# Optimization experiments

Hardware: AMD Instinct MI355X
Metric: run time of the kernel (lower is better)

The kernel has to match this reference:

```python
import jax, jax.numpy as jnp
import numpy as np

BLANK_ID = 0

def setup_inputs() -> dict:
    key = jax.random.key(0)
    k1, k2, k3, k4 = jax.random.split(key, 4)
    B, T, U, V = 4, 512, 100, 1024
    logits = jax.random.normal(k1, (B, T, U + 1, V), dtype=jnp.float32)
    labels = jax.random.randint(k2, (B, U), 0, V, dtype=jnp.int32)
    logit_lengths = jax.random.randint(k3, (B,), 0, T, dtype=jnp.int32)
    label_lengths = jax.random.randint(k4, (B,), 0, U, dtype=jnp.int32)
    return {"logits": logits, "labels": labels,
            "logit_lengths": logit_lengths, "label_lengths": label_lengths}


def _rnnt_alpha_final(logits, labels, logit_lengths, label_lengths):
    # logits: (B, T, U+1, V) treated as log-probs (as in the torch CPU path)
    B, T, Up1, V = logits.shape
    U = Up1 - 1
    dt = logits.dtype

    blank = logits[..., BLANK_ID]                                   # (B, T, U+1)
    # emit[b,t,u] = logits[b,t,u,labels[b,u]] for u in [0,U)
    emit = jnp.take_along_axis(logits[:, :, :U, :],
                               labels[:, None, :, None], axis=3)[..., 0]  # (B, T, U)

    zero_col = jnp.zeros((B, 1), dtype=dt)
    # Row t=0: alpha[0,u] = sum_{j<u} emit[0,j], alpha[0,0] = 0
    row0 = jnp.concatenate([zero_col, jnp.cumsum(emit[:, 0, :], axis=1)], axis=1)  # (B, U+1)

    def step(prev, xs):
        # prev: alpha row at t-1, shape (B, U+1)
        blank_tm1, emit_t = xs   # (B, U+1), (B, U)
        # Recurrence: row[u] = logaddexp(prev[u] + blank_tm1[u], row[u-1] + emit_t[u-1])
        # Linear log-domain recurrence solved with cumulative logsumexp:
        #   row[u] = C[u] + logcumsumexp(a - C)[u], a = prev + blank_tm1, C = prefix-sum of emit_t
        a = prev + blank_tm1
        C = jnp.concatenate([zero_col, jnp.cumsum(emit_t, axis=1)], axis=1)  # (B, U+1)
        row = C + jax.lax.cumlogsumexp(a - C, axis=1)
        return row, row

    xs = (jnp.swapaxes(blank[:, :-1, :], 0, 1),   # blank at t-1, for t = 1..T-1
          jnp.swapaxes(emit[:, 1:, :], 0, 1))     # emit at t,   for t = 1..T-1
    _, rows = jax.lax.scan(step, row0, xs)        # (T-1, B, U+1)
    alpha = jnp.concatenate([row0[None], rows], axis=0)  # (T, B, U+1)

    t_idx = logit_lengths - 1                     # alpha[T_b - 1, :]
    u_idx = label_lengths                         # column U_b
    per_sample = -alpha[t_idx, jnp.arange(B), u_idx]
    return per_sample


def reference(logits, labels, logit_lengths, label_lengths):
    V = logits.shape[-1]
    logit_lengths = jnp.clip(logit_lengths, 1, logits.shape[1])
    label_lengths = jnp.clip(label_lengths, 1, logits.shape[2] - 1)
    labels = jnp.clip(labels, 0, V - 1)
    per_sample = _rnnt_alpha_final(logits, labels, logit_lengths, label_lengths)
    # reduction = 'mean': sum over batch / batch_size, returned with shape (1,)
    return jnp.mean(per_sample).reshape(1)
```

## Files before the change

### kernel.cpp

```cpp
#include <hip/hip_runtime.h>


constexpr int B = 4, T = 512, U = 100, Up1 = 101, V = 1024;
constexpr int DIAGS = T + U;
constexpr int MM4 = (DIAGS + 3) / 4;
constexpr int W = 4;
constexpr float LOG2E = 1.44269504088896340736f;
constexpr float LN2 = 0.69314718055994530942f;

__device__ double2 g_D1[(size_t)B * MM4 * 64];
__device__ double2 g_D2[(size_t)B * MM4 * 64];
__device__ double2 g_D3[(size_t)B * MM4 * 64];
__device__ double2 g_D4[(size_t)B * MM4 * 64];
__device__ double2 g_D5[(size_t)B * MM4 * 64];
__device__ double2 g_L1[3][B * 64];
__device__ double2 g_L2[3][B * 64];
__device__ float g_mm[B * MM4];
__device__ float g_lastm[B][3];
__device__ float g_ps[B];
__device__ int g_ctr = 0;

__device__ __forceinline__ int clampi(int x, int lo, int hi) {
  return x < lo ? lo : (x > hi ? hi : x);
}
__device__ __forceinline__ float fexp2(float x) {
  float r; asm("v_exp_f32 %0, %1" : "=v"(r) : "v"(x)); return r;
}
__device__ __forceinline__ float flog2(float x) {
  float r; asm("v_log_f32 %0, %1" : "=v"(r) : "v"(x)); return r;
}
__device__ __forceinline__ double wave_shr1_f64(double x) {
  int hi = __double2hiint(x), lo = __double2loint(x);
  hi = __builtin_amdgcn_update_dpp(hi, hi, 0x138 , 0xF, 0xF, false);
  lo = __builtin_amdgcn_update_dpp(lo, lo, 0x138 , 0xF, 0xF, false);
  return __hiloint2double(hi, lo);
}

__global__ __launch_bounds__(256) void gather_kernel(const float* __restrict__ logits,
                                                     const int* __restrict__ labels,
                                                     const int* __restrict__ logit_len,
                                                     const int* __restrict__ label_len) {
  const int b = blockIdx.y;
  const int mr = blockIdx.x * 4 + (threadIdx.x >> 6);
  const int l = threadIdx.x & 63;
  if (mr >= MM4) return;
  const int Tb = clampi(logit_len[b], 1, T);
  const int Ub = clampi(label_len[b], 1, U);
  const int smax = Tb - 1 + Ub;
  const int Mq = smax >> 2, rem = smax & 3;

  const float* lg = logits + (size_t)b * T * Up1 * V;
  const int u0 = 2 * l, u1 = u0 + 1;
  int labz = 0, labw = 0;
  if (u0 >= 1 && u0 <= U) labz = clampi(labels[b * U + (u0 - 1)], 0, V - 1);
  if (u0 < U)             labw = clampi(labels[b * U + u0], 0, V - 1);

  if (mr >= Mq) {
    const size_t idx = ((size_t)b * MM4 + mr) * 64 + l;
    g_D1[idx] = make_double2(1.0, 0.0);
    g_D2[idx] = make_double2(0.0, 0.0);
    g_D3[idx] = make_double2(0.0, 1.0);
    g_D4[idx] = make_double2(0.0, 0.0);
    g_D5[idx] = make_double2(0.0, 0.0);
    if (l == 0) g_mm[b * MM4 + mr] = 0.f;

    if (mr == Mq) {
      for (int j = 0; j < rem; ++j) {
        int r = 4 * Mq + j;
        float vx = 0.f, vy = 0.f, vz = 0.f, vw = 0.f;
        bool bx = false, by = false, bz = false, bw = false;
        int tx = r - u0;
        if (u0 <= Ub && tx >= 0 && tx <= Tb - 1) { vx = LOG2E * lg[((size_t)tx * Up1 + u0) * V]; bx = true; }
        int ty = r - u1;
        if (u1 <= Ub && ty >= 0 && ty <= Tb - 1) { vy = LOG2E * lg[((size_t)ty * Up1 + u1) * V]; by = true; }
        int tz = r - u0 + 1;
        if (u0 >= 1 && u0 <= Ub && tz >= 0 && tz <= Tb - 1) { vz = LOG2E * lg[((size_t)tz * Up1 + (u0 - 1)) * V + labz]; bz = true; }
        int tw = r - u0;
        if (u0 <= Ub - 1 && tw >= 0 && tw <= Tb - 1) { vw = LOG2E * lg[((size_t)tw * Up1 + u0) * V + labw]; bw = true; }
        float s_ = (bx ? vx : 0.f) + (by ? vy : 0.f) + (bz ? vz : 0.f) + (bw ? vw : 0.f);
        float c_ = (float)((int)bx + (int)by + (int)bz + (int)bw);
        for (int off = 32; off; off >>= 1) { s_ += __shfl_xor(s_, off, 64); c_ += __shfl_xor(c_, off, 64); }
        float m = (c_ > 0.f) ? rintf(s_ / c_) : 0.f;
        g_L1[j][b * 64 + l] = make_double2(bx ? (double)fexp2(vx - m) : 0.0,
                                           bz ? (double)fexp2(vz - m) : 0.0);
        g_L2[j][b * 64 + l] = make_double2(by ? (double)fexp2(vy - m) : 0.0,
                                           bw ? (double)fexp2(vw - m) : 0.0);
        if (l == 0) g_lastm[b][j] = m;
      }
    }
    return;
  }

  float vx[4], vy[4], vz[4], vw[4];
  bool bx[4], by[4], bz[4], bw[4];
#pragma unroll
  for (int k = 0; k < 4; ++k) {
    int r = 4 * mr + k;
    vx[k] = vy[k] = vz[k] = vw[k] = 0.f;
    bx[k] = by[k] = bz[k] = bw[k] = false;
    int tx = r - u0;
    if (u0 <= Ub && tx >= 0 && tx <= Tb - 1) { vx[k] = LOG2E * lg[((size_t)tx * Up1 + u0) * V]; bx[k] = true; }
    int ty = r - u1;
    if (u1 <= Ub && ty >= 0 && ty <= Tb - 1) { vy[k] = LOG2E * lg[((size_t)ty * Up1 + u1) * V]; by[k] = true; }
    int tz = r - u0 + 1;
    if (u0 >= 1 && u0 <= Ub && tz >= 0 && tz <= Tb - 1) { vz[k] = LOG2E * lg[((size_t)tz * Up1 + (u0 - 1)) * V + labz]; bz[k] = true; }
    int tw = r - u0;
    if (u0 <= Ub - 1 && tw >= 0 && tw <= Tb - 1) { vw[k] = LOG2E * lg[((size_t)tw * Up1 + u0) * V + labw]; bw[k] = true; }
  }
  float s_ = 0.f, c_ = 0.f;
#pragma unroll
  for (int k = 0; k < 4; ++k) {
    s_ += (bx[k] ? vx[k] : 0.f) + (by[k] ? vy[k] : 0.f) +
          (bz[k] ? vz[k] : 0.f) + (bw[k] ? vw[k] : 0.f);
    c_ += (float)((int)bx[k] + (int)by[k] + (int)bz[k] + (int)bw[k]);
  }
  for (int off = 32; off; off >>= 1) { s_ += __shfl_xor(s_, off, 64); c_ += __shfl_xor(c_, off, 64); }
  const float m = (c_ > 0.f) ? rintf(s_ / c_) : 0.f;

  float fX[4], fY[4], fZ[4], fW[4];
#pragma unroll
  for (int k = 0; k < 4; ++k) {
    fX[k] = bx[k] ? fexp2(vx[k] - m) : 0.f;
    fY[k] = by[k] ? fexp2(vy[k] - m) : 0.f;
    fZ[k] = bz[k] ? fexp2(vz[k] - m) : 0.f;
    fW[k] = bw[k] ? fexp2(vw[k] - m) : 0.f;
  }

#define COMP2(P, Q, R_, S, Tc, Uc, i, jj)                                      \
  {                                                                            \
    float y1n = __shfl_up(fY[i], 1, 64);                                       \
    float w1n = __shfl_up(fW[i], 1, 64);                                       \
    double X1 = fX[i], Y1 = fY[i], Z1 = fZ[i], W1 = fW[i];                     \
    double X2 = fX[jj], Y2 = fY[jj], Z2 = fZ[jj], W2 = fW[jj];                 \
    P = X2 * X1; Q = X2 * Z1 + Z2 * (double)y1n; R_ = Z2 * (double)w1n;        \
    S = Y2 * Y1; Tc = W2 * X1 + Y2 * W1; Uc = W2 * Z1;                         \
  }
  double Mp, Mq_, Mr, Ms, Mt, Mu, Np, Nq, Nr, Ns, Nt, Nu;
  COMP2(Mp, Mq_, Mr, Ms, Mt, Mu, 0, 1);
  COMP2(Np, Nq, Nr, Ns, Nt, Nu, 2, 3);
#undef COMP2
  double Mp1 = __shfl_up(Mp, 1, 64), Mq1 = __shfl_up(Mq_, 1, 64);
  double Mr1 = __shfl_up(Mr, 1, 64), Ms1 = __shfl_up(Ms, 1, 64);
  double Mt1 = __shfl_up(Mt, 1, 64), Mu1 = __shfl_up(Mu, 1, 64);

  double dA  = Np * Mp;
  double dB1 = Np * Mq_ + Nq * Ms1;
  double dA1 = Np * Mr + Nq * Mt1 + Nr * Mp1;
  double dB2 = Nq * Mu1 + Nr * Mq1;
  double dA2 = Nr * Mr1;
  double eB  = Ns * Ms;
  double eA  = Ns * Mt + Nt * Mp;
  double eB1 = Ns * Mu + Nt * Mq_ + Nu * Ms1;
  double eA1 = Nt * Mr + Nu * Mt1;
  double eB2 = Nu * Mu1;

  const size_t idx = ((size_t)b * MM4 + mr) * 64 + l;
  g_D1[idx] = make_double2(dA, dB1);
  g_D2[idx] = make_double2(dA1, dB2);
  g_D3[idx] = make_double2(dA2, eB);
  g_D4[idx] = make_double2(eA, eB1);
  g_D5[idx] = make_double2(eA1, eB2);
  if (l == 0) g_mm[b * MM4 + mr] = 4.f * m;
}

__global__ __launch_bounds__(64, 1)
void dp_kernel(const int* __restrict__ logit_len,
               const int* __restrict__ label_len,
               float* __restrict__ out) {
  const int b = blockIdx.x;
  const int lane = threadIdx.x;
  const int Tb = clampi(logit_len[b], 1, T);
  const int Ub = clampi(label_len[b], 1, U);
  const int smax = Tb - 1 + Ub;
  const int Mq = smax >> 2, rem = smax & 3;
  const double2* D1 = g_D1 + (size_t)b * MM4 * 64 + lane;
  const double2* D2 = g_D2 + (size_t)b * MM4 * 64 + lane;
  const double2* D3 = g_D3 + (size_t)b * MM4 * 64 + lane;
  const double2* D4 = g_D4 + (size_t)b * MM4 * 64 + lane;
  const double2* D5 = g_D5 + (size_t)b * MM4 * 64 + lane;

  double A = (lane == 0) ? 1.0 : 0.0;
  double Bc = 0.0;

  double2 a1[W], a2[W], a3[W], a4[W], a5[W];
  double2 b1[W], b2[W], b3[W], b4[W], b5[W];
  double2 c1[W], c2[W], c3[W], c4[W], c5[W];

#define LOADG(u1_, u2_, u3_, u4_, u5_, grp)                                    \
  {                                                                            \
    const size_t o_ = (size_t)(grp) * (W * 64);                                \
    _Pragma("unroll")                                                          \
    for (int j_ = 0; j_ < W; ++j_) {                                           \
      u1_[j_] = D1[o_ + j_ * 64];                                              \
      u2_[j_] = D2[o_ + j_ * 64];                                              \
      u3_[j_] = D3[o_ + j_ * 64];                                              \
      u4_[j_] = D4[o_ + j_ * 64];                                              \
      u5_[j_] = D5[o_ + j_ * 64];                                              \
    }                                                                          \
  }

#define STEPS(u1_, u2_, u3_, u4_, u5_)                                         \
  {                                                                            \
    _Pragma("unroll")                                                          \
    for (int j_ = 0; j_ < W; ++j_) {                                           \
      double A1s = wave_shr1_f64(A);                                           \
      double B1s = wave_shr1_f64(Bc);                                          \
      double A2s = wave_shr1_f64(A1s);                                         \
      double B2s = wave_shr1_f64(B1s);                                         \
      double na = fma(A, u1_[j_].x, fma(B1s, u1_[j_].y,                        \
                   fma(A1s, u2_[j_].x, fma(B2s, u2_[j_].y,                     \
                       A2s * u3_[j_].x))));                                    \
      double nb = fma(Bc, u3_[j_].y, fma(A, u4_[j_].x,                         \
                   fma(B1s, u4_[j_].y, fma(A1s, u5_[j_].x,                     \
                       B2s * u5_[j_].y))));                                    \
      A = na; Bc = nb;                                                         \
    }                                                                          \
  }

  const int NWC = (Mq + W - 1) / W;
  if (NWC > 0) {
    LOADG(a1, a2, a3, a4, a5, 0);
    if (NWC > 1) LOADG(b1, b2, b3, b4, b5, 1);
    for (int k = 0; k < NWC; k += 3) {
      if (k + 2 < NWC) LOADG(c1, c2, c3, c4, c5, k + 2);
      STEPS(a1, a2, a3, a4, a5);
      if (k + 1 < NWC) {
        if (k + 3 < NWC) LOADG(a1, a2, a3, a4, a5, k + 3);
        STEPS(b1, b2, b3, b4, b5);
        if (k + 2 < NWC) {
          if (k + 4 < NWC) LOADG(b1, b2, b3, b4, b5, k + 4);
          STEPS(c1, c2, c3, c4, c5);
        }
      }
    }
  }
  for (int j = 0; j < rem; ++j) {
    double2 L1 = g_L1[j][b * 64 + lane];
    double2 L2 = g_L2[j][b * 64 + lane];
    double shrB = wave_shr1_f64(Bc);
    double na = fma(A, L1.x, shrB * L1.y);
    double nb = fma(Bc, L2.x, A * L2.y);
    A = na; Bc = nb;
  }

  const int ansLane = Ub >> 1;
  double va = __shfl(A, ansLane, 64);
  double vb = __shfl(Bc, ansLane, 64);
  double v = (Ub & 1) ? vb : va;
  int ev = ((__double2hiint(v) >> 20) & 0x7ff) - 1023;
  double mant = ldexp(v, -ev);

  float msum = 0.f;
  for (int mI = lane; mI < Mq; mI += 64) msum += g_mm[b * MM4 + mI];
  for (int off = 32; off; off >>= 1) msum += __shfl_xor(msum, off, 64);
  for (int j = 0; j < rem; ++j) msum += g_lastm[b][j];

  float lg2 = (float)ev + flog2((float)mant) + msum;

  if (lane == 0) {
    __hip_atomic_store(&g_ps[b], lg2, __ATOMIC_RELEASE, __HIP_MEMORY_SCOPE_AGENT);
    int old = __hip_atomic_fetch_add(&g_ctr, 1, __ATOMIC_ACQ_REL,
                                     __HIP_MEMORY_SCOPE_AGENT);
    if (old == B - 1) {
      float s = 0.0f;
      for (int i = 0; i < B; ++i)
        s += __hip_atomic_load(&g_ps[i], __ATOMIC_ACQUIRE, __HIP_MEMORY_SCOPE_AGENT);
      out[0] = -s * (LN2 / B);
      __hip_atomic_store(&g_ctr, 0, __ATOMIC_RELAXED, __HIP_MEMORY_SCOPE_AGENT);
    }
  }
#undef LOADG
#undef STEPS
}

extern "C" void kernel_launch(void* const* d_in, const int* in_sizes, int n_in,
                              void* d_out, int out_size, void* d_ws, size_t ws_size,
                              hipStream_t stream) {
  const float* logits = (const float*)d_in[0];
  const int* labels = (const int*)d_in[1];
  const int* logit_len = (const int*)d_in[2];
  const int* label_len = (const int*)d_in[3];
  float* out = (float*)d_out;

  hipLaunchKernelGGL(gather_kernel, dim3((MM4 + 3) / 4, B), dim3(256), 0, stream,
                     logits, labels, logit_len, label_len);
  hipLaunchKernelGGL(dp_kernel, dim3(B), dim3(64), 0, stream,
                     logit_len, label_len, out);
}
```

Measured before the change: 30.42 us.

## Compose eight anti-diagonal transfer steps per matrix in gather kernel

The gather kernel now multiplies two 4-step banded transfer operators into one 8-step operator, so each wave stores nine double2 coefficient arrays per eight diagonals instead of five per four. The sequential DP kernel then runs half as many dependent steps, each using wider shifts (up to four lanes) and a tree-shaped sum instead of an FMA chain. This shortens the serial critical path at the cost of more DPP shifts and multiplies per step, more register pressure from the prefetch buffers, and a larger remainder of up to seven single steps.

```diff
diff --git a/kernel.cpp b/kernel.cpp
--- a/kernel.cpp
+++ b/kernel.cpp
@@ -3,20 +3,24 @@
 
 constexpr int B = 4, T = 512, U = 100, Up1 = 101, V = 1024;
 constexpr int DIAGS = T + U;
-constexpr int MM4 = (DIAGS + 3) / 4;
-constexpr int W = 4;
+constexpr int MM8 = 78;
+constexpr int W = 3;
 constexpr float LOG2E = 1.44269504088896340736f;
 constexpr float LN2 = 0.69314718055994530942f;
 
-__device__ double2 g_D1[(size_t)B * MM4 * 64];
-__device__ double2 g_D2[(size_t)B * MM4 * 64];
-__device__ double2 g_D3[(size_t)B * MM4 * 64];
-__device__ double2 g_D4[(size_t)B * MM4 * 64];
-__device__ double2 g_D5[(size_t)B * MM4 * 64];
-__device__ double2 g_L1[3][B * 64];
-__device__ double2 g_L2[3][B * 64];
-__device__ float g_mm[B * MM4];
-__device__ float g_lastm[B][3];
+__device__ double2 g_G1[(size_t)B * MM8 * 64];
+__device__ double2 g_G2[(size_t)B * MM8 * 64];
+__device__ double2 g_G3[(size_t)B * MM8 * 64];
+__device__ double2 g_G4[(size_t)B * MM8 * 64];
+__device__ double2 g_G5[(size_t)B * MM8 * 64];
+__device__ double2 g_G6[(size_t)B * MM8 * 64];
+__device__ double2 g_G7[(size_t)B * MM8 * 64];
+__device__ double2 g_G8[(size_t)B * MM8 * 64];
+__device__ double2 g_G9[(size_t)B * MM8 * 64];
+__device__ double2 g_L1[7][B * 64];
+__device__ double2 g_L2[7][B * 64];
+__device__ float g_mm[B * MM8];
+__device__ float g_lastm[B][7];
 __device__ float g_ps[B];
 __device__ int g_ctr = 0;
 
@@ -43,11 +47,11 @@
   const int b = blockIdx.y;
   const int mr = blockIdx.x * 4 + (threadIdx.x >> 6);
   const int l = threadIdx.x & 63;
-  if (mr >= MM4) return;
+  if (mr >= MM8) return;
   const int Tb = clampi(logit_len[b], 1, T);
   const int Ub = clampi(label_len[b], 1, U);
   const int smax = Tb - 1 + Ub;
-  const int Mq = smax >> 2, rem = smax & 3;
+  const int Mq8 = smax >> 3, rem = smax & 7;
 
   const float* lg = logits + (size_t)b * T * Up1 * V;
   const int u0 = 2 * l, u1 = u0 + 1;
@@ -55,28 +59,37 @@
   if (u0 >= 1 && u0 <= U) labz = clampi(labels[b * U + (u0 - 1)], 0, V - 1);
   if (u0 < U)             labw = clampi(labels[b * U + u0], 0, V - 1);
 
-  if (mr >= Mq) {
-    const size_t idx = ((size_t)b * MM4 + mr) * 64 + l;
-    g_D1[idx] = make_double2(1.0, 0.0);
-    g_D2[idx] = make_double2(0.0, 0.0);
-    g_D3[idx] = make_double2(0.0, 1.0);
-    g_D4[idx] = make_double2(0.0, 0.0);
-    g_D5[idx] = make_double2(0.0, 0.0);
-    if (l == 0) g_mm[b * MM4 + mr] = 0.f;
-
-    if (mr == Mq) {
+#define RAWROW(r, vx, vy, vz, vw, bx, by, bz, bw)                              \
+  {                                                                            \
+    vx = vy = vz = vw = 0.f; bx = by = bz = bw = false;                        \
+    int tx = (r) - u0;                                                         \
+    if (u0 <= Ub && tx >= 0 && tx <= Tb - 1) { vx = LOG2E * lg[((size_t)tx * Up1 + u0) * V]; bx = true; } \
+    int ty = (r) - u1;                                                         \
+    if (u1 <= Ub && ty >= 0 && ty <= Tb - 1) { vy = LOG2E * lg[((size_t)ty * Up1 + u1) * V]; by = true; } \
+    int tz = (r) - u0 + 1;                                                     \
+    if (u0 >= 1 && u0 <= Ub && tz >= 0 && tz <= Tb - 1) { vz = LOG2E * lg[((size_t)tz * Up1 + (u0 - 1)) * V + labz]; bz = true; } \
+    int tw = (r) - u0;                                                         \
+    if (u0 <= Ub - 1 && tw >= 0 && tw <= Tb - 1) { vw = LOG2E * lg[((size_t)tw * Up1 + u0) * V + labw]; bw = true; } \
+  }
+
+  if (mr >= Mq8) {
+    const size_t idx = ((size_t)b * MM8 + mr) * 64 + l;
+    g_G1[idx] = make_double2(1.0, 0.0);
+    g_G2[idx] = make_double2(0.0, 0.0);
+    g_G3[idx] = make_double2(0.0, 0.0);
+    g_G4[idx] = make_double2(0.0, 0.0);
+    g_G5[idx] = make_double2(0.0, 0.0);
+    g_G6[idx] = make_double2(0.0, 0.0);
+    g_G7[idx] = make_double2(0.0, 1.0);
+    g_G8[idx] = make_double2(0.0, 0.0);
+    g_G9[idx] = make_double2(0.0, 0.0);
+    if (l == 0) g_mm[b * MM8 + mr] = 0.f;
+
+    if (mr == Mq8) {
       for (int j = 0; j < rem; ++j) {
-        int r = 4 * Mq + j;
-        float vx = 0.f, vy = 0.f, vz = 0.f, vw = 0.f;
-        bool bx = false, by = false, bz = false, bw = false;
-        int tx = r - u0;
-        if (u0 <= Ub && tx >= 0 && tx <= Tb - 1) { vx = LOG2E * lg[((size_t)tx * Up1 + u0) * V]; bx = true; }
-        int ty = r - u1;
-        if (u1 <= Ub && ty >= 0 && ty <= Tb - 1) { vy = LOG2E * lg[((size_t)ty * Up1 + u1) * V]; by = true; }
-        int tz = r - u0 + 1;
-        if (u0 >= 1 && u0 <= Ub && tz >= 0 && tz <= Tb - 1) { vz = LOG2E * lg[((size_t)tz * Up1 + (u0 - 1)) * V + labz]; bz = true; }
-        int tw = r - u0;
-        if (u0 <= Ub - 1 && tw >= 0 && tw <= Tb - 1) { vw = LOG2E * lg[((size_t)tw * Up1 + u0) * V + labw]; bw = true; }
+        int r = 8 * Mq8 + j;
+        float vx, vy, vz, vw; bool bx, by, bz, bw;
+        RAWROW(r, vx, vy, vz, vw, bx, by, bz, bw);
         float s_ = (bx ? vx : 0.f) + (by ? vy : 0.f) + (bz ? vz : 0.f) + (bw ? vw : 0.f);
         float c_ = (float)((int)bx + (int)by + (int)bz + (int)bw);
         for (int off = 32; off; off >>= 1) { s_ += __shfl_xor(s_, off, 64); c_ += __shfl_xor(c_, off, 64); }
@@ -91,25 +104,15 @@
     return;
   }
 
-  float vx[4], vy[4], vz[4], vw[4];
-  bool bx[4], by[4], bz[4], bw[4];
+  float vx[8], vy[8], vz[8], vw[8];
+  bool bx[8], by[8], bz[8], bw[8];
 #pragma unroll
-  for (int k = 0; k < 4; ++k) {
-    int r = 4 * mr + k;
-    vx[k] = vy[k] = vz[k] = vw[k] = 0.f;
-    bx[k] = by[k] = bz[k] = bw[k] = false;
-    int tx = r - u0;
-    if (u0 <= Ub && tx >= 0 && tx <= Tb - 1) { vx[k] = LOG2E * lg[((size_t)tx * Up1 + u0) * V]; bx[k] = true; }
-    int ty = r - u1;
-    if (u1 <= Ub && ty >= 0 && ty <= Tb - 1) { vy[k] = LOG2E * lg[((size_t)ty * Up1 + u1) * V]; by[k] = true; }
-    int tz = r - u0 + 1;
-    if (u0 >= 1 && u0 <= Ub && tz >= 0 && tz <= Tb - 1) { vz[k] = LOG2E * lg[((size_t)tz * Up1 + (u0 - 1)) * V + labz]; bz[k] = true; }
-    int tw = r - u0;
-    if (u0 <= Ub - 1 && tw >= 0 && tw <= Tb - 1) { vw[k] = LOG2E * lg[((size_t)tw * Up1 + u0) * V + labw]; bw[k] = true; }
-  }
+  for (int k = 0; k < 8; ++k)
+    RAWROW(8 * mr + k, vx[k], vy[k], vz[k], vw[k], bx[k], by[k], bz[k], bw[k]);
+
   float s_ = 0.f, c_ = 0.f;
 #pragma unroll
-  for (int k = 0; k < 4; ++k) {
+  for (int k = 0; k < 8; ++k) {
     s_ += (bx[k] ? vx[k] : 0.f) + (by[k] ? vy[k] : 0.f) +
           (bz[k] ? vz[k] : 0.f) + (bw[k] ? vw[k] : 0.f);
     c_ += (float)((int)bx[k] + (int)by[k] + (int)bz[k] + (int)bw[k]);
@@ -117,9 +120,9 @@
   for (int off = 32; off; off >>= 1) { s_ += __shfl_xor(s_, off, 64); c_ += __shfl_xor(c_, off, 64); }
   const float m = (c_ > 0.f) ? rintf(s_ / c_) : 0.f;
 
-  float fX[4], fY[4], fZ[4], fW[4];
+  float fX[8], fY[8], fZ[8], fW[8];
 #pragma unroll
-  for (int k = 0; k < 4; ++k) {
+  for (int k = 0; k < 8; ++k) {
     fX[k] = bx[k] ? fexp2(vx[k] - m) : 0.f;
     fY[k] = by[k] ? fexp2(vy[k] - m) : 0.f;
     fZ[k] = bz[k] ? fexp2(vz[k] - m) : 0.f;
@@ -135,32 +138,77 @@
     P = X2 * X1; Q = X2 * Z1 + Z2 * (double)y1n; R_ = Z2 * (double)w1n;        \
     S = Y2 * Y1; Tc = W2 * X1 + Y2 * W1; Uc = W2 * Z1;                         \
   }
-  double Mp, Mq_, Mr, Ms, Mt, Mu, Np, Nq, Nr, Ns, Nt, Nu;
-  COMP2(Mp, Mq_, Mr, Ms, Mt, Mu, 0, 1);
-  COMP2(Np, Nq, Nr, Ns, Nt, Nu, 2, 3);
+#define COMP4(aa0, aa1, aa2, ab1, ab2, ba0, ba1, bb0, bb1, bb2, i0)            \
+  {                                                                            \
+    double Mp, Mq_, Mr, Ms, Mt, Mu, Np, Nq, Nr, Ns, Nt, Nu;                    \
+    COMP2(Mp, Mq_, Mr, Ms, Mt, Mu, (i0), (i0) + 1);                            \
+    COMP2(Np, Nq, Nr, Ns, Nt, Nu, (i0) + 2, (i0) + 3);                         \
+    double Mp1 = __shfl_up(Mp, 1, 64), Mq1 = __shfl_up(Mq_, 1, 64);            \
+    double Mr1 = __shfl_up(Mr, 1, 64), Ms1 = __shfl_up(Ms, 1, 64);             \
+    double Mt1 = __shfl_up(Mt, 1, 64), Mu1 = __shfl_up(Mu, 1, 64);             \
+    aa0 = Np * Mp;                                                             \
+    ab1 = Np * Mq_ + Nq * Ms1;                                                 \
+    aa1 = Np * Mr + Nq * Mt1 + Nr * Mp1;                                       \
+    ab2 = Nq * Mu1 + Nr * Mq1;                                                 \
+    aa2 = Nr * Mr1;                                                            \
+    bb0 = Ns * Ms;                                                             \
+    ba0 = Ns * Mt + Nt * Mp;                                                   \
+    bb1 = Ns * Mu + Nt * Mq_ + Nu * Ms1;                                       \
+    ba1 = Nt * Mr + Nu * Mt1;                                                  \
+    bb2 = Nu * Mu1;                                                            \
+  }
+
+  double Maa0, Maa1, Maa2, Mab1, Mab2, Mba0, Mba1, Mbb0, Mbb1, Mbb2;
+  double Naa0, Naa1, Naa2, Nab1, Nab2, Nba0, Nba1, Nbb0, Nbb1, Nbb2;
+  COMP4(Maa0, Maa1, Maa2, Mab1, Mab2, Mba0, Mba1, Mbb0, Mbb1, Mbb2, 0);
+  COMP4(Naa0, Naa1, Naa2, Nab1, Nab2, Nba0, Nba1, Nbb0, Nbb1, Nbb2, 4);
+#undef COMP4
 #undef COMP2
-  double Mp1 = __shfl_up(Mp, 1, 64), Mq1 = __shfl_up(Mq_, 1, 64);
-  double Mr1 = __shfl_up(Mr, 1, 64), Ms1 = __shfl_up(Ms, 1, 64);
-  double Mt1 = __shfl_up(Mt, 1, 64), Mu1 = __shfl_up(Mu, 1, 64);
-
-  double dA  = Np * Mp;
-  double dB1 = Np * Mq_ + Nq * Ms1;
-  double dA1 = Np * Mr + Nq * Mt1 + Nr * Mp1;
-  double dB2 = Nq * Mu1 + Nr * Mq1;
-  double dA2 = Nr * Mr1;
-  double eB  = Ns * Ms;
-  double eA  = Ns * Mt + Nt * Mp;
-  double eB1 = Ns * Mu + Nt * Mq_ + Nu * Ms1;
-  double eA1 = Nt * Mr + Nu * Mt1;
-  double eB2 = Nu * Mu1;
-
-  const size_t idx = ((size_t)b * MM4 + mr) * 64 + l;
-  g_D1[idx] = make_double2(dA, dB1);
-  g_D2[idx] = make_double2(dA1, dB2);
-  g_D3[idx] = make_double2(dA2, eB);
-  g_D4[idx] = make_double2(eA, eB1);
-  g_D5[idx] = make_double2(eA1, eB2);
-  if (l == 0) g_mm[b * MM4 + mr] = 4.f * m;
+
+  double sMaa0_1 = __shfl_up(Maa0, 1, 64), sMaa0_2 = __shfl_up(Maa0, 2, 64);
+  double sMaa1_1 = __shfl_up(Maa1, 1, 64), sMaa1_2 = __shfl_up(Maa1, 2, 64);
+  double sMaa2_1 = __shfl_up(Maa2, 1, 64), sMaa2_2 = __shfl_up(Maa2, 2, 64);
+  double sMab1_1 = __shfl_up(Mab1, 1, 64), sMab1_2 = __shfl_up(Mab1, 2, 64);
+  double sMab2_1 = __shfl_up(Mab2, 1, 64), sMab2_2 = __shfl_up(Mab2, 2, 64);
+  double sMba0_1 = __shfl_up(Mba0, 1, 64), sMba0_2 = __shfl_up(Mba0, 2, 64);
+  double sMba1_1 = __shfl_up(Mba1, 1, 64), sMba1_2 = __shfl_up(Mba1, 2, 64);
+  double sMbb0_1 = __shfl_up(Mbb0, 1, 64), sMbb0_2 = __shfl_up(Mbb0, 2, 64);
+  double sMbb1_1 = __shfl_up(Mbb1, 1, 64), sMbb1_2 = __shfl_up(Mbb1, 2, 64);
+  double sMbb2_1 = __shfl_up(Mbb2, 1, 64), sMbb2_2 = __shfl_up(Mbb2, 2, 64);
+
+  double Paa0 = Naa0 * Maa0;
+  double Paa1 = Naa0 * Maa1 + Naa1 * sMaa0_1 + Nab1 * sMba0_1;
+  double Paa2 = Naa0 * Maa2 + Naa1 * sMaa1_1 + Naa2 * sMaa0_2 +
+                Nab1 * sMba1_1 + Nab2 * sMba0_2;
+  double Paa3 = Naa1 * sMaa2_1 + Naa2 * sMaa1_2 + Nab2 * sMba1_2;
+  double Paa4 = Naa2 * sMaa2_2;
+  double Pab1 = Naa0 * Mab1 + Nab1 * sMbb0_1;
+  double Pab2 = Naa0 * Mab2 + Naa1 * sMab1_1 + Nab1 * sMbb1_1 + Nab2 * sMbb0_2;
+  double Pab3 = Naa1 * sMab2_1 + Naa2 * sMab1_2 + Nab1 * sMbb2_1 + Nab2 * sMbb1_2;
+  double Pab4 = Naa2 * sMab2_2 + Nab2 * sMbb2_2;
+  double Pba0 = Nba0 * Maa0 + Nbb0 * Mba0;
+  double Pba1 = Nba0 * Maa1 + Nba1 * sMaa0_1 + Nbb0 * Mba1 + Nbb1 * sMba0_1;
+  double Pba2 = Nba0 * Maa2 + Nba1 * sMaa1_1 + Nbb1 * sMba1_1 + Nbb2 * sMba0_2;
+  double Pba3 = Nba1 * sMaa2_1 + Nbb2 * sMba1_2;
+  double Pbb0 = Nbb0 * Mbb0;
+  double Pbb1 = Nba0 * Mab1 + Nbb0 * Mbb1 + Nbb1 * sMbb0_1;
+  double Pbb2 = Nba0 * Mab2 + Nba1 * sMab1_1 + Nbb0 * Mbb2 + Nbb1 * sMbb1_1 +
+                Nbb2 * sMbb0_2;
+  double Pbb3 = Nba1 * sMab2_1 + Nbb1 * sMbb2_1 + Nbb2 * sMbb1_2;
+  double Pbb4 = Nbb2 * sMbb2_2;
+
+  const size_t idx = ((size_t)b * MM8 + mr) * 64 + l;
+  g_G1[idx] = make_double2(Paa0, Paa1);
+  g_G2[idx] = make_double2(Paa2, Paa3);
+  g_G3[idx] = make_double2(Paa4, Pab1);
+  g_G4[idx] = make_double2(Pab2, Pab3);
+  g_G5[idx] = make_double2(Pab4, Pba0);
+  g_G6[idx] = make_double2(Pba1, Pba2);
+  g_G7[idx] = make_double2(Pba3, Pbb0);
+  g_G8[idx] = make_double2(Pbb1, Pbb2);
+  g_G9[idx] = make_double2(Pbb3, Pbb4);
+  if (l == 0) g_mm[b * MM8 + mr] = 8.f * m;
+#undef RAWROW
 }
 
 __global__ __launch_bounds__(64, 1)
@@ -172,34 +220,38 @@
   const int Tb = clampi(logit_len[b], 1, T);
   const int Ub = clampi(label_len[b], 1, U);
   const int smax = Tb - 1 + Ub;
-  const int Mq = smax >> 2, rem = smax & 3;
-  const double2* D1 = g_D1 + (size_t)b * MM4 * 64 + lane;
-  const double2* D2 = g_D2 + (size_t)b * MM4 * 64 + lane;
-  const double2* D3 = g_D3 + (size_t)b * MM4 * 64 + lane;
-  const double2* D4 = g_D4 + (size_t)b * MM4 * 64 + lane;
-  const double2* D5 = g_D5 + (size_t)b * MM4 * 64 + lane;
+  const int Mq8 = smax >> 3, rem = smax & 7;
+  const double2* G1 = g_G1 + (size_t)b * MM8 * 64 + lane;
+  const double2* G2 = g_G2 + (size_t)b * MM8 * 64 + lane;
+  const double2* G3 = g_G3 + (size_t)b * MM8 * 64 + lane;
+  const double2* G4 = g_G4 + (size_t)b * MM8 * 64 + lane;
+  const double2* G5 = g_G5 + (size_t)b * MM8 * 64 + lane;
+  const double2* G6 = g_G6 + (size_t)b * MM8 * 64 + lane;
+  const double2* G7 = g_G7 + (size_t)b * MM8 * 64 + lane;
+  const double2* G8 = g_G8 + (size_t)b * MM8 * 64 + lane;
+  const double2* G9 = g_G9 + (size_t)b * MM8 * 64 + lane;
 
   double A = (lane == 0) ? 1.0 : 0.0;
   double Bc = 0.0;
 
-  double2 a1[W], a2[W], a3[W], a4[W], a5[W];
-  double2 b1[W], b2[W], b3[W], b4[W], b5[W];
-  double2 c1[W], c2[W], c3[W], c4[W], c5[W];
-
-#define LOADG(u1_, u2_, u3_, u4_, u5_, grp)                                    \
+  double2 a1[W], a2[W], a3[W], a4[W], a5[W], a6[W], a7[W], a8[W], a9[W];
+  double2 b1[W], b2[W], b3[W], b4[W], b5[W], b6[W], b7[W], b8[W], b9[W];
+  double2 c1[W], c2[W], c3[W], c4[W], c5[W], c6[W], c7[W], c8[W], c9[W];
+
+#define LOADG(u1_, u2_, u3_, u4_, u5_, u6_, u7_, u8_, u9_, grp)                \
   {                                                                            \
     const size_t o_ = (size_t)(grp) * (W * 64);                                \
     _Pragma("unroll")                                                          \
     for (int j_ = 0; j_ < W; ++j_) {                                           \
-      u1_[j_] = D1[o_ + j_ * 64];                                              \
-      u2_[j_] = D2[o_ + j_ * 64];                                              \
-      u3_[j_] = D3[o_ + j_ * 64];                                              \
-      u4_[j_] = D4[o_ + j_ * 64];                                              \
-      u5_[j_] = D5[o_ + j_ * 64];                                              \
+      u1_[j_] = G1[o_ + j_ * 64]; u2_[j_] = G2[o_ + j_ * 64];                  \
+      u3_[j_] = G3[o_ + j_ * 64]; u4_[j_] = G4[o_ + j_ * 64];                  \
+      u5_[j_] = G5[o_ + j_ * 64]; u6_[j_] = G6[o_ + j_ * 64];                  \
+      u7_[j_] = G7[o_ + j_ * 64]; u8_[j_] = G8[o_ + j_ * 64];                  \
+      u9_[j_] = G9[o_ + j_ * 64];                                              \
     }                                                                          \
   }
 
-#define STEPS(u1_, u2_, u3_, u4_, u5_)                                         \
+#define STEPS(u1_, u2_, u3_, u4_, u5_, u6_, u7_, u8_, u9_)                     \
   {                                                                            \
     _Pragma("unroll")                                                          \
     for (int j_ = 0; j_ < W; ++j_) {                                           \
@@ -207,29 +259,37 @@
       double B1s = wave_shr1_f64(Bc);                                          \
       double A2s = wave_shr1_f64(A1s);                                         \
       double B2s = wave_shr1_f64(B1s);                                         \
-      double na = fma(A, u1_[j_].x, fma(B1s, u1_[j_].y,                        \
-                   fma(A1s, u2_[j_].x, fma(B2s, u2_[j_].y,                     \
-                       A2s * u3_[j_].x))));                                    \
-      double nb = fma(Bc, u3_[j_].y, fma(A, u4_[j_].x,                         \
-                   fma(B1s, u4_[j_].y, fma(A1s, u5_[j_].x,                     \
-                       B2s * u5_[j_].y))));                                    \
+      double A3s = wave_shr1_f64(A2s);                                         \
+      double B3s = wave_shr1_f64(B2s);                                         \
+      double A4s = wave_shr1_f64(A3s);                                         \
+      double B4s = wave_shr1_f64(B3s);                                         \
+      double na = ((A * u1_[j_].x + A1s * u1_[j_].y) +                         \
+                   (A2s * u2_[j_].x + A3s * u2_[j_].y)) +                      \
+                  ((A4s * u3_[j_].x + B1s * u3_[j_].y) +                       \
+                   (B2s * u4_[j_].x + B3s * u4_[j_].y)) +                      \
+                  B4s * u5_[j_].x;                                             \
+      double nb = ((A * u5_[j_].y + A1s * u6_[j_].x) +                         \
+                   (A2s * u6_[j_].y + A3s * u7_[j_].x)) +                      \
+                  ((Bc * u7_[j_].y + B1s * u8_[j_].x) +                        \
+                   (B2s * u8_[j_].y + B3s * u9_[j_].x)) +                      \
+                  B4s * u9_[j_].y;                                             \
       A = na; Bc = nb;                                                         \
     }                                                                          \
   }
 
-  const int NWC = (Mq + W - 1) / W;
+  const int NWC = (Mq8 + W - 1) / W;
   if (NWC > 0) {
-    LOADG(a1, a2, a3, a4, a5, 0);
-    if (NWC > 1) LOADG(b1, b2, b3, b4, b5, 1);
+    LOADG(a1, a2, a3, a4, a5, a6, a7, a8, a9, 0);
+    if (NWC > 1) LOADG(b1, b2, b3, b4, b5, b6, b7, b8, b9, 1);
     for (int k = 0; k < NWC; k += 3) {
-      if (k + 2 < NWC) LOADG(c1, c2, c3, c4, c5, k + 2);
-      STEPS(a1, a2, a3, a4, a5);
+      if (k + 2 < NWC) LOADG(c1, c2, c3, c4, c5, c6, c7, c8, c9, k + 2);
+      STEPS(a1, a2, a3, a4, a5, a6, a7, a8, a9);
       if (k + 1 < NWC) {
-        if (k + 3 < NWC) LOADG(a1, a2, a3, a4, a5, k + 3);
-        STEPS(b1, b2, b3, b4, b5);
+        if (k + 3 < NWC) LOADG(a1, a2, a3, a4, a5, a6, a7, a8, a9, k + 3);
+        STEPS(b1, b2, b3, b4, b5, b6, b7, b8, b9);
         if (k + 2 < NWC) {
-          if (k + 4 < NWC) LOADG(b1, b2, b3, b4, b5, k + 4);
-          STEPS(c1, c2, c3, c4, c5);
+          if (k + 4 < NWC) LOADG(b1, b2, b3, b4, b5, b6, b7, b8, b9, k + 4);
+          STEPS(c1, c2, c3, c4, c5, c6, c7, c8, c9);
         }
       }
     }
@@ -251,7 +311,7 @@
   double mant = ldexp(v, -ev);
 
   float msum = 0.f;
-  for (int mI = lane; mI < Mq; mI += 64) msum += g_mm[b * MM4 + mI];
+  for (int mI = lane; mI < Mq8; mI += 64) msum += g_mm[b * MM8 + mI];
   for (int off = 32; off; off >>= 1) msum += __shfl_xor(msum, off, 64);
   for (int j = 0; j < rem; ++j) msum += g_lastm[b][j];
 
@@ -282,7 +342,7 @@
   const int* label_len = (const int*)d_in[3];
   float* out = (float*)d_out;
 
-  hipLaunchKernelGGL(gather_kernel, dim3((MM4 + 3) / 4, B), dim3(256), 0, stream,
+  hipLaunchKernelGGL(gather_kernel, dim3((MM8 + 3) / 4, B), dim3(256), 0, stream,
                      logits, labels, logit_len, label_len);
   hipLaunchKernelGGL(dp_kernel, dim3(B), dim3(64), 0, stream,
                      logit_len, label_len, out);
```

Result: slower. 38.60 us (+26.9%).
